# Optimization experiments

Measured on AMD Instinct MI355X. Metric: run time of the kernel, lower is better.

## Reference

```python
import jax, jax.numpy as jnp
import numpy as np

# Model constants matching init_kwargs
C1, C2, FS, IMG = 1024, 3, 16, 128
NF = FS * FS                     # n_features = 256 (== pos_out_dim)
L = C1 // NF                     # 4 hypernetwork-generated layers
WD = NF + (L - 1) * NF + L       # weight_dim = 1028
M = NF // 4                      # 64 frequencies per coord dim
SIGMA = 10.0
B = 8


def _coords_pe(b):
    """get_coords([IMG, IMG]) + positional_encoding, flattened to [b, IMG*IMG, NF]."""
    v0, v1 = -0.99999, 1.0
    r = (v1 - v0) / (2 * IMG)
    seq = v0 + r + 2 * r * jnp.arange(IMG, dtype=jnp.float32)
    gy, gx = jnp.meshgrid(seq, seq, indexing='ij')
    coords = jnp.stack([gy, gx], axis=-1)                 # [IMG, IMG, 2]
    j = jnp.arange(M, dtype=jnp.float32)
    coeffs = 2.0 * jnp.pi * (SIGMA ** (j / M))            # [M]
    vp = coeffs * coords[..., None]                       # [IMG, IMG, 2, M]
    pe = jnp.concatenate([jnp.cos(vp), jnp.sin(vp)], -1)  # [IMG, IMG, 2, 2M]
    pe = pe.reshape(IMG, IMG, 4 * M)                      # flatten(-2,-1)
    x2 = pe.reshape(1, IMG * IMG, NF)
    return jnp.broadcast_to(x2, (b, IMG * IMG, NF))


def setup_inputs() -> dict:
    key = jax.random.key(0)
    ks = jax.random.split(key, 5)
    std = 0.001  # matches _initialize_weights
    x = jax.random.normal(ks[0], (B, C1, FS, FS), jnp.float32)
    conv_w = std * jax.random.normal(ks[1], (C1 + L, C1), jnp.float32)  # 1x1 conv kernel
    conv_b = jnp.zeros((C1 + L,), jnp.float32)
    wfine_w = std * jax.random.normal(ks[2], (NF, NF), jnp.float32)
    wfine_b = jnp.zeros((NF,), jnp.float32)
    last1_w = std * jax.random.normal(ks[3], (C2, NF), jnp.float32)
    last1_b = jnp.zeros((C2,), jnp.float32)
    prelu_a = jnp.array(0.25, jnp.float32)  # nn.PReLU default single param
    return {"x": x, "conv_w": conv_w, "conv_b": conv_b,
            "wfine_w": wfine_w, "wfine_b": wfine_b,
            "last1_w": last1_w, "last1_b": last1_b, "prelu_a": prelu_a}


def reference(x, conv_w, conv_b, wfine_w, wfine_b, last1_w, last1_b, prelu_a):
    b = x.shape[0]
    x2 = _coords_pe(b)  # [b, N_px, NF]
    # 1x1 conv == channel matmul
    x1 = jnp.einsum('bchw,oc->bohw', x, conv_w) + conv_b[None, :, None, None]
    W = x1.reshape(b, WD, NF)
    W = jnp.einsum('bik,jk->bij', W, wfine_w) + wfine_b  # W_fine linear
    out = x2
    for j in range(L):
        wj = W[:, NF * j + j: NF * (j + 1) + j, :]           # [b, NF, NF]
        bj = W[:, NF * (j + 1) + j: NF * (j + 1) + j + 1, :]  # [b, 1, NF]
        h = jnp.einsum('bij,bjk->bik', out, wj) + bj
        out = jnp.where(h >= 0, h, prelu_a * h)              # PReLU
    out = jnp.einsum('bik,ck->bic', out, last1_w) + last1_b  # last1
    out = jax.nn.silu(out)                                   # SiLU
    out = out.transpose(0, 2, 1).reshape(b, C2, IMG, IMG)
    return out
```

## Files before the change

### kernel.cpp

```cpp
#include <hip/hip_runtime.h>
#include <hip/hip_fp16.h>
#include <math.h>

typedef _Float16 f16;
typedef _Float16 f16x4 __attribute__((ext_vector_type(4)));
typedef _Float16 f16x8 __attribute__((ext_vector_type(8)));
typedef float f32x4 __attribute__((ext_vector_type(4)));

#define MFMA16(a, b, c) __builtin_amdgcn_mfma_f32_16x16x32_f16((a), (b), (c), 0, 0, 0)

static constexpr float SW_W   = 1024.f;
static constexpr float SA_A   = 64.f;
static constexpr float SA1_s  = 16.f;
static constexpr float INV_SW    = 1.f / 1024.f;
static constexpr float INV_SASW  = 1.f / (64.f * 1024.f);
static constexpr float INV_SA1SW = 1.f / (16.f * 1024.f);

static constexpr size_t OFF_CY = 0;
static constexpr size_t OFF_CX = OFF_CY + 128 * 128 * 4;
static constexpr size_t OFF_LW = OFF_CX + 128 * 128 * 4;
static constexpr size_t OFF_XT = OFF_LW + 16 * 256 * 2;
static constexpr size_t OFF_X1 = OFF_XT + (size_t)8 * 256 * 1024 * 2;
static constexpr size_t OFF_W  = OFF_X1 + (size_t)8 * 1028 * 256 * 2;
static constexpr size_t OFF_AY = OFF_W  + (size_t)8 * 1028 * 256 * 4;
static constexpr size_t OFF_BX = OFF_AY + (size_t)8 * 128 * 256 * 2;
static constexpr size_t OFF_WT = OFF_BX + (size_t)8 * 128 * 256 * 2;

static __device__ inline f32x4 zero4() { f32x4 v = {0.f, 0.f, 0.f, 0.f}; return v; }

__global__ void k_prep(const float* __restrict__ x, f16* __restrict__ xT,
                       float* __restrict__ cy, float* __restrict__ cx,
                       f16* __restrict__ lwf, const float* __restrict__ lw)
{
    __shared__ float tile[64][65];
    const int bid = blockIdx.x;
    const int t = threadIdx.x;
    if (bid < 512) {
        const int b = bid >> 6;
        const int ct = (bid >> 2) & 15;
        const int nt = bid & 3;
        const int c0 = ct << 6, n0 = nt << 6;
        for (int i = 0; i < 16; i++) {
            int e = i * 256 + t;
            int cc = e >> 6, nn = e & 63;
            tile[cc][nn] = x[(size_t)((b << 10) + c0 + cc) * 256 + n0 + nn];
        }
        __syncthreads();
        for (int i = 0; i < 16; i++) {
            int e = i * 256 + t;
            int nn = e >> 6, cc = e & 63;
            xT[(size_t)((b << 8) + n0 + nn) * 1024 + c0 + cc] = (f16)tile[cc][nn];
        }
        return;
    }
    int id = (bid - 512) * 256 + t;
    const float r = 1.99999f / 256.f;
    if (id < 32768) {
        float* dst = (id < 16384) ? cy : cx;
        int e = id & 16383;
        int row = e >> 7, f = e & 127;
        float s = -0.99999f + r + 2.f * r * (float)row;
        float coef = 6.283185307179586f * powf(10.f, (float)(f & 63) * (1.f / 64.f));
        float arg = coef * s;
        dst[e] = (f < 64) ? cosf(arg) : sinf(arg);
    } else if (id < 33280) {
        int id2 = id - 32768;
        int c = id2 >> 6, lane = id2 & 63;
        int nlo = lane & 15, q4 = lane >> 4;
        f16x8 v;
        #pragma unroll
        for (int ko = 0; ko < 8; ko++)
            v[ko] = (nlo < 3) ? (f16)(lw[nlo * 256 + (c << 5) + (q4 << 3) + ko] * SW_W) : (f16)0.f;
        *(f16x8*)(lwf + id2 * 8) = v;
    }
}

template <int MODE>
__global__ __launch_bounds__(256, 4) void k_gemm(
    const float* __restrict__ Af32, const f16* __restrict__ Af16,
    const f16* __restrict__ Bf16, const float* __restrict__ Bf32,
    f16* __restrict__ out16, float* __restrict__ outW,
    const float* __restrict__ bias)
{
    constexpr int NC = MODE ? 8 : 32;
    __shared__ __align__(16) f16 Ab[2][64 * 32];
    __shared__ __align__(16) f16 Bb[2][64 * 32];
    const int t = threadIdx.x;
    const int lane = t & 63;
    const int wc = t >> 6;
    const int nlo = lane & 15, q4 = lane >> 4;
    const int blk = blockIdx.x;
    const int b = blk / 68;
    const int rem = blk % 68;
    const int m0 = (rem >> 2) << 6;
    const int n0 = (rem & 3) << 6;
    const int srow = t >> 2, sk = (t & 3) << 3;

    auto stageA = [&](int buf, int k0) {
        const int m = m0 + srow;
        f16x8 v;
        if (m < 1028) {
            if constexpr (MODE == 0) {
                const float* src = Af32 + (size_t)m * 1024 + k0 + sk;
                #pragma unroll
                for (int i = 0; i < 8; i++) v[i] = (f16)(src[i] * SW_W);
            } else {
                v = *(const f16x8*)(Af16 + (size_t)(b * 1028 + m) * 256 + k0 + sk);
            }
        } else {
            #pragma unroll
            for (int i = 0; i < 8; i++) v[i] = (f16)0.f;
        }
        *(f16x8*)(&Ab[buf][t << 3]) = v;
    };
    auto stageB = [&](int buf, int k0) {
        const int n = n0 + srow;
        f16x8 v;
        if constexpr (MODE == 0) {
            v = *(const f16x8*)(Bf16 + (size_t)((b << 8) + n) * 1024 + k0 + sk);
        } else {
            const float* src = Bf32 + (size_t)n * 256 + k0 + sk;
            #pragma unroll
            for (int i = 0; i < 8; i++) v[i] = (f16)(src[i] * SW_W);
        }
        *(f16x8*)(&Bb[buf][t << 3]) = v;
    };

    f32x4 acc[4];
    #pragma unroll
    for (int mt = 0; mt < 4; mt++) acc[mt] = zero4();

    stageA(0, 0); stageB(0, 0);
    __syncthreads();
    for (int c = 0; c < NC; c++) {
        const int cb = c & 1;
        if (c + 1 < NC) { stageA(cb ^ 1, (c + 1) << 5); stageB(cb ^ 1, (c + 1) << 5); }
        f16x8 af[4], bf;
        bf = *(const f16x8*)(&Bb[cb][(((wc << 4) + nlo) << 5) + (q4 << 3)]);
        #pragma unroll
        for (int mt = 0; mt < 4; mt++)
            af[mt] = *(const f16x8*)(&Ab[cb][(((mt << 4) + nlo) << 5) + (q4 << 3)]);
        #pragma unroll
        for (int mt = 0; mt < 4; mt++)
            acc[mt] = MFMA16(af[mt], bf, acc[mt]);
        __syncthreads();
    }
    const int nn = n0 + (wc << 4) + nlo;
    #pragma unroll
    for (int mt = 0; mt < 4; mt++) {
        #pragma unroll
        for (int i = 0; i < 4; i++) {
            const int m = m0 + (mt << 4) + (q4 << 2) + i;
            if (m < 1028) {
                if constexpr (MODE == 0) {
                    float v = (acc[mt][i] * INV_SW + bias[m]) * SA1_s;
                    out16[(size_t)(b * 1028 + m) * 256 + nn] = (f16)v;
                } else {
                    outW[(size_t)(b * 1028 + m) * 256 + nn] =
                        acc[mt][i] * INV_SA1SW + bias[nn];
                }
            }
        }
    }
}

__global__ void k_wprep(const float* __restrict__ cy, const float* __restrict__ cx,
                        const float* __restrict__ W, f16* __restrict__ ayF,
                        f16* __restrict__ bxF, f16* __restrict__ wjT)
{
    __shared__ float tile[64][65];
    const int bid = blockIdx.x;
    const int t = threadIdx.x;
    if (bid < 256) {
        const int b = bid >> 5, which = (bid >> 4) & 1, rtile = bid & 15;
        const int r0 = rtile << 3;
        const float* ctab = which ? cx : cy;
        const float* Wb = W + (size_t)(b * 1028 + (which ? 128 : 0)) * 256;
        float acc[8];
        #pragma unroll
        for (int r = 0; r < 8; r++) acc[r] = 0.f;
        for (int k = 0; k < 128; k++) {
            const float wv = Wb[(k << 8) + t];
            #pragma unroll
            for (int r = 0; r < 8; r++)
                acc[r] = fmaf(ctab[((r0 + r) << 7) + k], wv, acc[r]);
        }
        const float b1v = which ? 0.f : W[(size_t)(b * 1028 + 256) * 256 + t];
        f16* dst = which ? bxF : ayF;
        for (int r = 0; r < 8; r++)
            dst[(size_t)((b << 7) + r0 + r) * 256 + t] = (f16)((acc[r] + b1v) * SA_A);
        return;
    }
    const int id = bid - 256;
    const int b = id / 48;
    const int rr = id % 48;
    const int jj = rr / 16;
    const int tt = rr % 16;
    const int kt = tt >> 2, wt = tt & 3;
    const int k0 = kt << 6, n0 = wt << 6;
    const float* src = W + (size_t)(b * 1028 + 257 * (jj + 1)) * 256;
    for (int i = 0; i < 16; i++) {
        int e = i * 256 + t;
        int kk = e >> 6, nn = e & 63;
        tile[kk][nn] = src[(size_t)(k0 + kk) * 256 + n0 + nn];
    }
    __syncthreads();
    f16* dst = wjT + (size_t)(b * 3 + jj) * 65536;
    #pragma unroll
    for (int i = 0; i < 2; i++) {
        const int g = i * 256 + t;
        const int c_rel = g >> 8, sub = g & 255;
        const int nt = sub >> 6, ln = sub & 63;
        const int nl = ln & 15, q4g = ln >> 4;
        f16x8 v;
        #pragma unroll
        for (int ko = 0; ko < 8; ko++)
            v[ko] = (f16)(tile[(c_rel << 5) + (q4g << 3) + ko][(nt << 4) + nl] * SW_W);
        const int c = (kt << 1) + c_rel;
        *(f16x8*)(dst + (size_t)(((((c << 2) | wt) << 2) | nt) << 9) + (ln << 3)) = v;
    }
}

__global__ __launch_bounds__(256, 3) void k_main(
    const f16* __restrict__ wjT, const float* __restrict__ Wfull,
    const f16* __restrict__ ayF, const f16* __restrict__ bxF,
    const f16* __restrict__ lwf, const float* __restrict__ lb,
    const float* __restrict__ pa_p, float* __restrict__ out)
{
    __shared__ __align__(16) unsigned char actS[32768];
    const int t = threadIdx.x;
    const int lane = t & 63;
    const int wc = t >> 6;
    const int nlo = lane & 15, q4 = lane >> 4;
    const int blk = blockIdx.x;
    const int b = blk & 7, rt = blk >> 3;
    const int p0 = rt << 6;
    const int y = p0 >> 7, x0 = p0 & 127;
    const float pa = pa_p[0];

    {
        const int r = t & 63, g = t >> 6;
        const f16* ayr = ayF + (size_t)((b << 7) + y) * 256;
        const f16* bxr = bxF + (size_t)((b << 7) + x0 + r) * 256;
        const int rx = r & 7;
        #pragma unroll
        for (int mm = 0; mm < 8; mm++) {
            const int slot = (g << 3) + mm;
            const int f0 = slot << 3;
            f16x8 av = *(const f16x8*)(ayr + f0);
            f16x8 bv = *(const f16x8*)(bxr + f0);
            f16x8 v;
            #pragma unroll
            for (int i = 0; i < 8; i++) {
                float hv = (float)av[i] + (float)bv[i];
                hv = fmaxf(hv, 0.f) + pa * fminf(hv, 0.f);
                v[i] = (f16)hv;
            }
            *(f16x8*)(actS + (r << 9) + ((slot ^ rx) << 4)) = v;
        }
    }
    __syncthreads();

    for (int jj = 0; jj < 3; jj++) {
        const f16* wl = wjT + (size_t)(b * 3 + jj) * 65536;
        auto loadB = [&](f16x8* dstv, int c) {
            const f16* p = wl + (size_t)(((c << 2) | wc) << 11) + (lane << 3);
            #pragma unroll
            for (int nt = 0; nt < 4; nt++)
                dstv[nt] = *(const f16x8*)(p + (nt << 9));
        };
        f32x4 acc[4][4];
        #pragma unroll
        for (int pt = 0; pt < 4; pt++)
            #pragma unroll
            for (int nt = 0; nt < 4; nt++) acc[pt][nt] = zero4();

        f16x8 bfA[4], bfB[4];
        loadB(bfA, 0);
        #pragma unroll
        for (int c = 0; c < 8; c++) {
            f16x8* cur = (c & 1) ? bfB : bfA;
            f16x8* nxt = (c & 1) ? bfA : bfB;
            if (c < 7) loadB(nxt, c + 1);
            const int sl = (c << 2) + q4;
            f16x8 af[4];
            #pragma unroll
            for (int pt = 0; pt < 4; pt++) {
                const int rr = (pt << 4) + nlo;
                af[pt] = *(const f16x8*)(actS + (rr << 9) + ((sl ^ (rr & 7)) << 4));
            }
            #pragma unroll
            for (int pt = 0; pt < 4; pt++)
                #pragma unroll
                for (int nt = 0; nt < 4; nt++)
                    acc[pt][nt] = MFMA16(cur[nt], af[pt], acc[pt][nt]);
        }
        __syncthreads();

        const float* bias = Wfull + (size_t)(b * 1028 + 257 * (jj + 1) + 256) * 256;
        #pragma unroll
        for (int nt = 0; nt < 4; nt++) {
            const int nb = (wc << 6) + (nt << 4) + (q4 << 2);
            const f32x4 b4 = *(const f32x4*)(bias + nb);
            #pragma unroll
            for (int pt = 0; pt < 4; pt++) {
                const int rr = (pt << 4) + nlo;
                f16x4 pk;
                #pragma unroll
                for (int i = 0; i < 4; i++) {
                    float v = acc[pt][nt][i] * INV_SW + b4[i] * SA_A;
                    v = fmaxf(v, 0.f) + pa * fminf(v, 0.f);
                    pk[i] = (f16)v;
                }
                *(f16x4*)(actS + (rr << 9) + (((nb >> 3) ^ (rr & 7)) << 4) + ((nb & 7) << 1)) = pk;
            }
        }
        __syncthreads();
    }

    {
        f32x4 acc2 = zero4();
        const int rr = (wc << 4) + nlo;
        #pragma unroll
        for (int c = 0; c < 8; c++) {
            const int sl = (c << 2) + q4;
            const f16x8 af = *(const f16x8*)(actS + (rr << 9) + ((sl ^ (rr & 7)) << 4));
            const f16x8 lf = *(const f16x8*)(lwf + (((c << 6) + lane) << 3));
            acc2 = MFMA16(af, lf, acc2);
        }
        if (nlo < 3) {
            const float lbv = lb[nlo];
            float* ob = out + ((size_t)(b * 3 + nlo) << 14) + p0 + (wc << 4) + (q4 << 2);
            #pragma unroll
            for (int i = 0; i < 4; i++) {
                float z = acc2[i] * INV_SASW + lbv;
                ob[i] = z / (1.f + expf(-z));
            }
        }
    }
}

extern "C" void kernel_launch(void* const* d_in, const int* in_sizes, int n_in,
                              void* d_out, int out_size, void* d_ws, size_t ws_size,
                              hipStream_t stream)
{
    (void)in_sizes; (void)n_in; (void)out_size; (void)ws_size;
    const float* x       = (const float*)d_in[0];
    const float* conv_w  = (const float*)d_in[1];
    const float* conv_b  = (const float*)d_in[2];
    const float* wfine_w = (const float*)d_in[3];
    const float* wfine_b = (const float*)d_in[4];
    const float* last1_w = (const float*)d_in[5];
    const float* last1_b = (const float*)d_in[6];
    const float* prelu_a = (const float*)d_in[7];
    char* ws = (char*)d_ws;
    float* Cy  = (float*)(ws + OFF_CY);
    float* Cx  = (float*)(ws + OFF_CX);
    f16*   lwf = (f16*)(ws + OFF_LW);
    f16*   xT  = (f16*)(ws + OFF_XT);
    f16*   x1  = (f16*)(ws + OFF_X1);
    float* W   = (float*)(ws + OFF_W);
    f16*   AyF = (f16*)(ws + OFF_AY);
    f16*   BxF = (f16*)(ws + OFF_BX);
    f16*   wjT = (f16*)(ws + OFF_WT);

    k_prep<<<642, 256, 0, stream>>>(x, xT, Cy, Cx, lwf, last1_w);
    k_gemm<0><<<544, 256, 0, stream>>>(conv_w, nullptr, xT, nullptr, x1, nullptr, conv_b);
    k_gemm<1><<<544, 256, 0, stream>>>(nullptr, x1, nullptr, wfine_w, nullptr, W, wfine_b);
    k_wprep<<<640, 256, 0, stream>>>(Cy, Cx, W, AyF, BxF, wjT);
    k_main<<<2048, 256, 0, stream>>>(wjT, W, AyF, BxF, lwf, last1_b, prelu_a, (float*)d_out);
}
```

Before: 124.2 us.

## Fuse conv and W_fine GEMMs into one kernel with pre-converted fp16 weights

Merges the two GEMM kernels into one k_fused kernel. Each block computes a 64-row by 256-column x1 tile, keeps it in shared memory, and applies W_fine directly, so the x1 intermediate never goes to global memory. conv_w and wfine_w are converted to fp16 once in k_prep (wfine_w in MFMA fragment layout), which removes per-tile fp32 conversion. In k_main, the weight prefetch now runs across layer boundaries and the bias loads are hoisted. The catch is that the fused kernel launches only 136 blocks on a large GPU, so parallelism is low and each block does more serial work.

Measured after the change: 114.2 us. 1.09x faster.

```diff
diff --git a/kernel.cpp b/kernel.cpp
--- a/kernel.cpp
+++ b/kernel.cpp
@@ -20,8 +20,9 @@
 static constexpr size_t OFF_CX = OFF_CY + 128 * 128 * 4;
 static constexpr size_t OFF_LW = OFF_CX + 128 * 128 * 4;
 static constexpr size_t OFF_XT = OFF_LW + 16 * 256 * 2;
-static constexpr size_t OFF_X1 = OFF_XT + (size_t)8 * 256 * 1024 * 2;
-static constexpr size_t OFF_W  = OFF_X1 + (size_t)8 * 1028 * 256 * 2;
+static constexpr size_t OFF_CW = OFF_XT + (size_t)8 * 256 * 1024 * 2;
+static constexpr size_t OFF_WF = OFF_CW + (size_t)1088 * 1024 * 2;
+static constexpr size_t OFF_W  = OFF_WF + 256 * 256 * 2;
 static constexpr size_t OFF_AY = OFF_W  + (size_t)8 * 1028 * 256 * 4;
 static constexpr size_t OFF_BX = OFF_AY + (size_t)8 * 128 * 256 * 2;
 static constexpr size_t OFF_WT = OFF_BX + (size_t)8 * 128 * 256 * 2;
@@ -30,7 +31,9 @@
 
 __global__ void k_prep(const float* __restrict__ x, f16* __restrict__ xT,
                        float* __restrict__ cy, float* __restrict__ cx,
-                       f16* __restrict__ lwf, const float* __restrict__ lw)
+                       f16* __restrict__ lwf, const float* __restrict__ lw,
+                       const float* __restrict__ cw, f16* __restrict__ cw16,
+                       const float* __restrict__ wf, f16* __restrict__ wf16)
 {
     __shared__ float tile[64][65];
     const int bid = blockIdx.x;
@@ -53,112 +56,174 @@
         }
         return;
     }
-    int id = (bid - 512) * 256 + t;
-    const float r = 1.99999f / 256.f;
-    if (id < 32768) {
-        float* dst = (id < 16384) ? cy : cx;
-        int e = id & 16383;
-        int row = e >> 7, f = e & 127;
-        float s = -0.99999f + r + 2.f * r * (float)row;
-        float coef = 6.283185307179586f * powf(10.f, (float)(f & 63) * (1.f / 64.f));
-        float arg = coef * s;
-        dst[e] = (f < 64) ? cosf(arg) : sinf(arg);
-    } else if (id < 33280) {
-        int id2 = id - 32768;
-        int c = id2 >> 6, lane = id2 & 63;
-        int nlo = lane & 15, q4 = lane >> 4;
+    if (bid < 642) {
+        int id = (bid - 512) * 256 + t;
+        const float r = 1.99999f / 256.f;
+        if (id < 32768) {
+            float* dst = (id < 16384) ? cy : cx;
+            int e = id & 16383;
+            int row = e >> 7, f = e & 127;
+            float s = -0.99999f + r + 2.f * r * (float)row;
+            float coef = 6.283185307179586f * powf(10.f, (float)(f & 63) * (1.f / 64.f));
+            float arg = coef * s;
+            dst[e] = (f < 64) ? cosf(arg) : sinf(arg);
+        } else if (id < 33280) {
+            int id2 = id - 32768;
+            int c = id2 >> 6, lane = id2 & 63;
+            int nlo = lane & 15, q4 = lane >> 4;
+            f16x8 v;
+            #pragma unroll
+            for (int ko = 0; ko < 8; ko++)
+                v[ko] = (nlo < 3) ? (f16)(lw[nlo * 256 + (c << 5) + (q4 << 3) + ko] * SW_W) : (f16)0.f;
+            *(f16x8*)(lwf + id2 * 8) = v;
+        }
+        return;
+    }
+    if (bid < 1186) {
+        const int g8 = (bid - 642) * 256 + t;
+        const int row = g8 >> 7, col0 = (g8 & 127) << 3;
         f16x8 v;
+        if (row < 1028) {
+            const float* src = cw + (size_t)row * 1024 + col0;
+            #pragma unroll
+            for (int i = 0; i < 8; i++) v[i] = (f16)(src[i] * SW_W);
+        } else {
+            #pragma unroll
+            for (int i = 0; i < 8; i++) v[i] = (f16)0.f;
+        }
+        *(f16x8*)(cw16 + (size_t)g8 * 8) = v;
+        return;
+    }
+    {
+        const int gg = (bid - 1186) * 256 + t;
+        const int lane = gg & 63, nt = (gg >> 6) & 3, wt = (gg >> 8) & 3, c = gg >> 10;
+        const int nlo = lane & 15, q4 = lane >> 4;
+        const int n = (wt << 6) + (nt << 4) + nlo;
+        f16x8 v;
         #pragma unroll
         for (int ko = 0; ko < 8; ko++)
-            v[ko] = (nlo < 3) ? (f16)(lw[nlo * 256 + (c << 5) + (q4 << 3) + ko] * SW_W) : (f16)0.f;
-        *(f16x8*)(lwf + id2 * 8) = v;
+            v[ko] = (f16)(wf[(size_t)n * 256 + (c << 5) + (q4 << 3) + ko] * SW_W);
+        *(f16x8*)(wf16 + (size_t)gg * 8) = v;
     }
 }
 
-template <int MODE>
-__global__ __launch_bounds__(256, 4) void k_gemm(
-    const float* __restrict__ Af32, const f16* __restrict__ Af16,
-    const f16* __restrict__ Bf16, const float* __restrict__ Bf32,
-    f16* __restrict__ out16, float* __restrict__ outW,
-    const float* __restrict__ bias)
+__global__ __launch_bounds__(256, 2) void k_fused(
+    const f16* __restrict__ cw16, const f16* __restrict__ xT,
+    const f16* __restrict__ wf16, const float* __restrict__ conv_b,
+    const float* __restrict__ wfine_b, float* __restrict__ W)
 {
-    constexpr int NC = MODE ? 8 : 32;
     __shared__ __align__(16) f16 Ab[2][64 * 32];
-    __shared__ __align__(16) f16 Bb[2][64 * 32];
+    __shared__ __align__(16) f16 Bb[2][256 * 32];
+    __shared__ __align__(16) unsigned char x1S[32768];
     const int t = threadIdx.x;
     const int lane = t & 63;
     const int wc = t >> 6;
     const int nlo = lane & 15, q4 = lane >> 4;
-    const int blk = blockIdx.x;
-    const int b = blk / 68;
-    const int rem = blk % 68;
-    const int m0 = (rem >> 2) << 6;
-    const int n0 = (rem & 3) << 6;
-    const int srow = t >> 2, sk = (t & 3) << 3;
+    const int b = blockIdx.x & 7, mtile = blockIdx.x >> 3;
+    const int m0 = mtile << 6;
 
     auto stageA = [&](int buf, int k0) {
-        const int m = m0 + srow;
-        f16x8 v;
-        if (m < 1028) {
-            if constexpr (MODE == 0) {
-                const float* src = Af32 + (size_t)m * 1024 + k0 + sk;
-                #pragma unroll
-                for (int i = 0; i < 8; i++) v[i] = (f16)(src[i] * SW_W);
-            } else {
-                v = *(const f16x8*)(Af16 + (size_t)(b * 1028 + m) * 256 + k0 + sk);
-            }
-        } else {
-            #pragma unroll
-            for (int i = 0; i < 8; i++) v[i] = (f16)0.f;
-        }
-        *(f16x8*)(&Ab[buf][t << 3]) = v;
+        *(f16x8*)(&Ab[buf][t << 3]) =
+            *(const f16x8*)(cw16 + (size_t)(m0 + (t >> 2)) * 1024 + k0 + ((t & 3) << 3));
     };
     auto stageB = [&](int buf, int k0) {
-        const int n = n0 + srow;
-        f16x8 v;
-        if constexpr (MODE == 0) {
-            v = *(const f16x8*)(Bf16 + (size_t)((b << 8) + n) * 1024 + k0 + sk);
-        } else {
-            const float* src = Bf32 + (size_t)n * 256 + k0 + sk;
-            #pragma unroll
-            for (int i = 0; i < 8; i++) v[i] = (f16)(src[i] * SW_W);
-        }
-        *(f16x8*)(&Bb[buf][t << 3]) = v;
+        #pragma unroll
+        for (int i = 0; i < 4; i++)
+            *(f16x8*)(&Bb[buf][(i * 256 + t) << 3]) =
+                *(const f16x8*)(xT + (size_t)((b << 8) + (i << 6) + (t >> 2)) * 1024 + k0 + ((t & 3) << 3));
     };
 
-    f32x4 acc[4];
+    f32x4 acc1[4][4];
     #pragma unroll
-    for (int mt = 0; mt < 4; mt++) acc[mt] = zero4();
+    for (int pt = 0; pt < 4; pt++)
+        #pragma unroll
+        for (int mc = 0; mc < 4; mc++) acc1[pt][mc] = zero4();
 
     stageA(0, 0); stageB(0, 0);
     __syncthreads();
-    for (int c = 0; c < NC; c++) {
+    for (int c = 0; c < 32; c++) {
         const int cb = c & 1;
-        if (c + 1 < NC) { stageA(cb ^ 1, (c + 1) << 5); stageB(cb ^ 1, (c + 1) << 5); }
-        f16x8 af[4], bf;
-        bf = *(const f16x8*)(&Bb[cb][(((wc << 4) + nlo) << 5) + (q4 << 3)]);
-        #pragma unroll
-        for (int mt = 0; mt < 4; mt++)
-            af[mt] = *(const f16x8*)(&Ab[cb][(((mt << 4) + nlo) << 5) + (q4 << 3)]);
-        #pragma unroll
-        for (int mt = 0; mt < 4; mt++)
-            acc[mt] = MFMA16(af[mt], bf, acc[mt]);
+        if (c + 1 < 32) { stageA(cb ^ 1, (c + 1) << 5); stageB(cb ^ 1, (c + 1) << 5); }
+        f16x8 bf[4], af[4];
+        #pragma unroll
+        for (int pt = 0; pt < 4; pt++)
+            bf[pt] = *(const f16x8*)(&Bb[cb][((wc << 8) + (((pt << 4) + nlo) << 2) + q4) << 3]);
+        #pragma unroll
+        for (int mc = 0; mc < 4; mc++)
+            af[mc] = *(const f16x8*)(&Ab[cb][(((((mc << 4) + nlo) << 2) + q4)) << 3]);
+        #pragma unroll
+        for (int pt = 0; pt < 4; pt++)
+            #pragma unroll
+            for (int mc = 0; mc < 4; mc++)
+                acc1[pt][mc] = MFMA16(bf[pt], af[mc], acc1[pt][mc]);
         __syncthreads();
     }
-    const int nn = n0 + (wc << 4) + nlo;
+
+    {
+        float cbv[4];
+        #pragma unroll
+        for (int mc = 0; mc < 4; mc++) {
+            const int m = m0 + (mc << 4) + nlo;
+            cbv[mc] = (m < 1028) ? conv_b[m] : 0.f;
+        }
+        #pragma unroll
+        for (int pt = 0; pt < 4; pt++) {
+            const int p0 = (wc << 6) + (pt << 4) + (q4 << 2);
+            #pragma unroll
+            for (int mc = 0; mc < 4; mc++) {
+                const int r = (mc << 4) + nlo;
+                f16x4 pk;
+                #pragma unroll
+                for (int i = 0; i < 4; i++)
+                    pk[i] = (f16)((acc1[pt][mc][i] * INV_SW + cbv[mc]) * SA1_s);
+                *(f16x4*)(x1S + (r << 9) + (((p0 >> 3) ^ (r & 7)) << 4) + ((p0 & 7) << 1)) = pk;
+            }
+        }
+    }
+    __syncthreads();
+
+    f32x4 acc2[4][4];
     #pragma unroll
-    for (int mt = 0; mt < 4; mt++) {
-        #pragma unroll
-        for (int i = 0; i < 4; i++) {
-            const int m = m0 + (mt << 4) + (q4 << 2) + i;
+    for (int mc = 0; mc < 4; mc++)
+        #pragma unroll
+        for (int jt = 0; jt < 4; jt++) acc2[mc][jt] = zero4();
+
+    auto loadW = [&](f16x8* d, int c2) {
+        const f16* p = wf16 + (size_t)((((c2 << 2) | wc)) << 11) + (lane << 3);
+        #pragma unroll
+        for (int jt = 0; jt < 4; jt++) d[jt] = *(const f16x8*)(p + (jt << 9));
+    };
+    f16x8 wfA[4], wfB[4];
+    loadW(wfA, 0);
+    #pragma unroll
+    for (int c2 = 0; c2 < 8; c2++) {
+        f16x8* cur = (c2 & 1) ? wfB : wfA;
+        f16x8* nxt = (c2 & 1) ? wfA : wfB;
+        if (c2 < 7) loadW(nxt, c2 + 1);
+        f16x8 af2[4];
+        #pragma unroll
+        for (int mc = 0; mc < 4; mc++) {
+            const int r = (mc << 4) + nlo;
+            af2[mc] = *(const f16x8*)(x1S + (r << 9) + ((((c2 << 2) + q4) ^ (r & 7)) << 4));
+        }
+        #pragma unroll
+        for (int mc = 0; mc < 4; mc++)
+            #pragma unroll
+            for (int jt = 0; jt < 4; jt++)
+                acc2[mc][jt] = MFMA16(cur[jt], af2[mc], acc2[mc][jt]);
+    }
+    #pragma unroll
+    for (int jt = 0; jt < 4; jt++) {
+        const int j0 = (wc << 6) + (jt << 4) + (q4 << 2);
+        const f32x4 b4 = *(const f32x4*)(wfine_b + j0);
+        #pragma unroll
+        for (int mc = 0; mc < 4; mc++) {
+            const int m = m0 + (mc << 4) + nlo;
             if (m < 1028) {
-                if constexpr (MODE == 0) {
-                    float v = (acc[mt][i] * INV_SW + bias[m]) * SA1_s;
-                    out16[(size_t)(b * 1028 + m) * 256 + nn] = (f16)v;
-                } else {
-                    outW[(size_t)(b * 1028 + m) * 256 + nn] =
-                        acc[mt][i] * INV_SA1SW + bias[nn];
-                }
+                f32x4 o;
+                #pragma unroll
+                for (int i = 0; i < 4; i++) o[i] = acc2[mc][jt][i] * INV_SA1SW + b4[i];
+                *(f32x4*)(W + ((size_t)(b * 1028 + m) << 8) + j0) = o;
             }
         }
     }
@@ -238,6 +303,16 @@
     const int y = p0 >> 7, x0 = p0 & 127;
     const float pa = pa_p[0];
 
+    const f16* wl0 = wjT + (size_t)(b * 3) * 65536;
+    auto loadBg = [&](f16x8* dstv, int g) {
+        const f16* p = wl0 + (size_t)(g >> 3) * 65536 + ((size_t)((((g & 7) << 2) | wc)) << 11) + (lane << 3);
+        #pragma unroll
+        for (int nt = 0; nt < 4; nt++) dstv[nt] = *(const f16x8*)(p + (nt << 9));
+    };
+
+    f16x8 bfA[4], bfB[4];
+    loadBg(bfA, 0);
+
     {
         const int r = t & 63, g = t >> 6;
         const f16* ayr = ayF + (size_t)((b << 7) + y) * 256;
@@ -262,26 +337,24 @@
     __syncthreads();
 
     for (int jj = 0; jj < 3; jj++) {
-        const f16* wl = wjT + (size_t)(b * 3 + jj) * 65536;
-        auto loadB = [&](f16x8* dstv, int c) {
-            const f16* p = wl + (size_t)(((c << 2) | wc) << 11) + (lane << 3);
-            #pragma unroll
-            for (int nt = 0; nt < 4; nt++)
-                dstv[nt] = *(const f16x8*)(p + (nt << 9));
-        };
+        const float* bias = Wfull + (size_t)(b * 1028 + 257 * (jj + 1) + 256) * 256;
+        f32x4 bias4[4];
+        #pragma unroll
+        for (int nt = 0; nt < 4; nt++)
+            bias4[nt] = *(const f32x4*)(bias + (wc << 6) + (nt << 4) + (q4 << 2));
+
         f32x4 acc[4][4];
         #pragma unroll
         for (int pt = 0; pt < 4; pt++)
             #pragma unroll
             for (int nt = 0; nt < 4; nt++) acc[pt][nt] = zero4();
 
-        f16x8 bfA[4], bfB[4];
-        loadB(bfA, 0);
         #pragma unroll
         for (int c = 0; c < 8; c++) {
-            f16x8* cur = (c & 1) ? bfB : bfA;
-            f16x8* nxt = (c & 1) ? bfA : bfB;
-            if (c < 7) loadB(nxt, c + 1);
+            const int g = jj * 8 + c;
+            f16x8* cur = (g & 1) ? bfB : bfA;
+            f16x8* nxt = (g & 1) ? bfA : bfB;
+            if (g < 23) loadBg(nxt, g + 1);
             const int sl = (c << 2) + q4;
             f16x8 af[4];
             #pragma unroll
@@ -297,18 +370,16 @@
         }
         __syncthreads();
 
-        const float* bias = Wfull + (size_t)(b * 1028 + 257 * (jj + 1) + 256) * 256;
         #pragma unroll
         for (int nt = 0; nt < 4; nt++) {
             const int nb = (wc << 6) + (nt << 4) + (q4 << 2);
-            const f32x4 b4 = *(const f32x4*)(bias + nb);
             #pragma unroll
             for (int pt = 0; pt < 4; pt++) {
                 const int rr = (pt << 4) + nlo;
                 f16x4 pk;
                 #pragma unroll
                 for (int i = 0; i < 4; i++) {
-                    float v = acc[pt][nt][i] * INV_SW + b4[i] * SA_A;
+                    float v = acc[pt][nt][i] * INV_SW + bias4[nt][i] * SA_A;
                     v = fmaxf(v, 0.f) + pa * fminf(v, 0.f);
                     pk[i] = (f16)v;
                 }
@@ -358,15 +429,15 @@
     float* Cx  = (float*)(ws + OFF_CX);
     f16*   lwf = (f16*)(ws + OFF_LW);
     f16*   xT  = (f16*)(ws + OFF_XT);
-    f16*   x1  = (f16*)(ws + OFF_X1);
+    f16*   cw16= (f16*)(ws + OFF_CW);
+    f16*   wf16= (f16*)(ws + OFF_WF);
     float* W   = (float*)(ws + OFF_W);
     f16*   AyF = (f16*)(ws + OFF_AY);
     f16*   BxF = (f16*)(ws + OFF_BX);
     f16*   wjT = (f16*)(ws + OFF_WT);
 
-    k_prep<<<642, 256, 0, stream>>>(x, xT, Cy, Cx, lwf, last1_w);
-    k_gemm<0><<<544, 256, 0, stream>>>(conv_w, nullptr, xT, nullptr, x1, nullptr, conv_b);
-    k_gemm<1><<<544, 256, 0, stream>>>(nullptr, x1, nullptr, wfine_w, nullptr, W, wfine_b);
+    k_prep<<<1218, 256, 0, stream>>>(x, xT, Cy, Cx, lwf, last1_w, conv_w, cw16, wfine_w, wf16);
+    k_fused<<<136, 256, 0, stream>>>(cw16, xT, wf16, conv_b, wfine_b, W);
     k_wprep<<<640, 256, 0, stream>>>(Cy, Cx, W, AyF, BxF, wjT);
     k_main<<<2048, 256, 0, stream>>>(wjT, W, AyF, BxF, lwf, last1_b, prelu_a, (float*)d_out);
 }
```

## Reassociate conv and W_fine GEMMs, prefetch weights across layers in main kernel

Applied to the files above, without the earlier changes.

The two front GEMMs are reassociated as conv_w·(x·wfine_wᵀ) instead of (conv_w·x)·wfine_wᵀ. The per-batch x·wfine product is computed first, and the bias term is folded in analytically as conv_b·rowsum(wfine) + wfine_b. This removes the x transpose pass and lets the weights be converted to f16 once in the prep kernel. In the main kernel, hypernetwork weight fragments are now prefetched across layer boundaries, activation fragments from LDS are double-buffered, and MFMA blocks are wrapped in s_setprio. The intermediate is rounded to f16 without a scale factor, which risks precision loss, and the extra register buffers may reduce occupancy.

Measured after the change: 143.9 us. 1.16x slower.

```diff
diff --git a/kernel.cpp b/kernel.cpp
--- a/kernel.cpp
+++ b/kernel.cpp
@@ -9,80 +9,94 @@
 
 #define MFMA16(a, b, c) __builtin_amdgcn_mfma_f32_16x16x32_f16((a), (b), (c), 0, 0, 0)
 
-static constexpr float SW_W   = 1024.f;
-static constexpr float SA_A   = 64.f;
-static constexpr float SA1_s  = 16.f;
-static constexpr float INV_SW    = 1.f / 1024.f;
-static constexpr float INV_SASW  = 1.f / (64.f * 1024.f);
-static constexpr float INV_SA1SW = 1.f / (16.f * 1024.f);
+static constexpr float SW_W    = 1024.f;
+static constexpr float SA_A    = 64.f;
+static constexpr float INV_SW  = 1.f / 1024.f;
+static constexpr float INV_SW2 = 1.f / (1024.f * 1024.f);
+static constexpr float INV_SASW = 1.f / (64.f * 1024.f);
 
 static constexpr size_t OFF_CY = 0;
-static constexpr size_t OFF_CX = OFF_CY + 128 * 128 * 4;
-static constexpr size_t OFF_LW = OFF_CX + 128 * 128 * 4;
-static constexpr size_t OFF_XT = OFF_LW + 16 * 256 * 2;
-static constexpr size_t OFF_X1 = OFF_XT + (size_t)8 * 256 * 1024 * 2;
-static constexpr size_t OFF_W  = OFF_X1 + (size_t)8 * 1028 * 256 * 2;
+static constexpr size_t OFF_CX = OFF_CY + 65536;
+static constexpr size_t OFF_LW = OFF_CX + 65536;
+static constexpr size_t OFF_S  = OFF_LW + 8192;
+static constexpr size_t OFF_CW = OFF_S  + 1024;
+static constexpr size_t OFF_WF = OFF_CW + (size_t)1088 * 1024 * 2;
+static constexpr size_t OFF_M2 = OFF_WF + 131072;
+static constexpr size_t OFF_W  = OFF_M2 + (size_t)8 * 256 * 1024 * 2;
 static constexpr size_t OFF_AY = OFF_W  + (size_t)8 * 1028 * 256 * 4;
 static constexpr size_t OFF_BX = OFF_AY + (size_t)8 * 128 * 256 * 2;
 static constexpr size_t OFF_WT = OFF_BX + (size_t)8 * 128 * 256 * 2;
 
 static __device__ inline f32x4 zero4() { f32x4 v = {0.f, 0.f, 0.f, 0.f}; return v; }
 
-__global__ void k_prep(const float* __restrict__ x, f16* __restrict__ xT,
-                       float* __restrict__ cy, float* __restrict__ cx,
-                       f16* __restrict__ lwf, const float* __restrict__ lw)
-{
-    __shared__ float tile[64][65];
+__global__ void k_prep(float* __restrict__ cy, float* __restrict__ cx,
+                       f16* __restrict__ lwf, const float* __restrict__ lw,
+                       const float* __restrict__ cw, f16* __restrict__ cw16,
+                       const float* __restrict__ wf, f16* __restrict__ wf16,
+                       float* __restrict__ S)
+{
     const int bid = blockIdx.x;
     const int t = threadIdx.x;
-    if (bid < 512) {
-        const int b = bid >> 6;
-        const int ct = (bid >> 2) & 15;
-        const int nt = bid & 3;
-        const int c0 = ct << 6, n0 = nt << 6;
-        for (int i = 0; i < 16; i++) {
-            int e = i * 256 + t;
-            int cc = e >> 6, nn = e & 63;
-            tile[cc][nn] = x[(size_t)((b << 10) + c0 + cc) * 256 + n0 + nn];
-        }
-        __syncthreads();
-        for (int i = 0; i < 16; i++) {
-            int e = i * 256 + t;
-            int nn = e >> 6, cc = e & 63;
-            xT[(size_t)((b << 8) + n0 + nn) * 1024 + c0 + cc] = (f16)tile[cc][nn];
+    if (bid < 130) {
+        int id = bid * 256 + t;
+        const float r = 1.99999f / 256.f;
+        if (id < 32768) {
+            float* dst = (id < 16384) ? cy : cx;
+            int e = id & 16383;
+            int row = e >> 7, f = e & 127;
+            float s = -0.99999f + r + 2.f * r * (float)row;
+            float coef = 6.283185307179586f * powf(10.f, (float)(f & 63) * (1.f / 64.f));
+            float arg = coef * s;
+            dst[e] = (f < 64) ? cosf(arg) : sinf(arg);
+        } else {
+            int id2 = id - 32768;
+            int c = id2 >> 6, lane = id2 & 63;
+            int nlo = lane & 15, q4 = lane >> 4;
+            f16x8 v;
+            #pragma unroll
+            for (int ko = 0; ko < 8; ko++)
+                v[ko] = (nlo < 3) ? (f16)(lw[nlo * 256 + (c << 5) + (q4 << 3) + ko] * SW_W) : (f16)0.f;
+            *(f16x8*)(lwf + id2 * 8) = v;
         }
         return;
     }
-    int id = (bid - 512) * 256 + t;
-    const float r = 1.99999f / 256.f;
-    if (id < 32768) {
-        float* dst = (id < 16384) ? cy : cx;
-        int e = id & 16383;
-        int row = e >> 7, f = e & 127;
-        float s = -0.99999f + r + 2.f * r * (float)row;
-        float coef = 6.283185307179586f * powf(10.f, (float)(f & 63) * (1.f / 64.f));
-        float arg = coef * s;
-        dst[e] = (f < 64) ? cosf(arg) : sinf(arg);
-    } else if (id < 33280) {
-        int id2 = id - 32768;
-        int c = id2 >> 6, lane = id2 & 63;
-        int nlo = lane & 15, q4 = lane >> 4;
+    if (bid < 674) {
+        const int g8 = (bid - 130) * 256 + t;
+        const int row = g8 >> 7, col0 = (g8 & 127) << 3;
         f16x8 v;
-        #pragma unroll
-        for (int ko = 0; ko < 8; ko++)
-            v[ko] = (nlo < 3) ? (f16)(lw[nlo * 256 + (c << 5) + (q4 << 3) + ko] * SW_W) : (f16)0.f;
-        *(f16x8*)(lwf + id2 * 8) = v;
-    }
-}
-
-template <int MODE>
-__global__ __launch_bounds__(256, 4) void k_gemm(
-    const float* __restrict__ Af32, const f16* __restrict__ Af16,
-    const f16* __restrict__ Bf16, const float* __restrict__ Bf32,
-    f16* __restrict__ out16, float* __restrict__ outW,
-    const float* __restrict__ bias)
-{
-    constexpr int NC = MODE ? 8 : 32;
+        if (row < 1028) {
+            const float* src = cw + (size_t)row * 1024 + col0;
+            #pragma unroll
+            for (int i = 0; i < 8; i++) v[i] = (f16)(src[i] * SW_W);
+        } else {
+            #pragma unroll
+            for (int i = 0; i < 8; i++) v[i] = (f16)0.f;
+        }
+        *(f16x8*)(cw16 + (size_t)g8 * 8) = v;
+        return;
+    }
+    if (bid < 706) {
+        const int gg = (bid - 674) * 256 + t;
+        const int row = gg >> 5, col0 = (gg & 31) << 3;
+        const float* src = wf + (size_t)row * 256 + col0;
+        f16x8 v;
+        #pragma unroll
+        for (int i = 0; i < 8; i++) v[i] = (f16)(src[i] * SW_W);
+        *(f16x8*)(wf16 + (size_t)gg * 8) = v;
+        return;
+    }
+    {
+        const float* src = wf + (size_t)t * 256;
+        float s = 0.f;
+        for (int k = 0; k < 256; k++) s += src[k];
+        S[t] = s;
+    }
+}
+
+__global__ __launch_bounds__(256, 4) void k_gemmA(
+    const float* __restrict__ x, const f16* __restrict__ wf16,
+    f16* __restrict__ M2)
+{
     __shared__ __align__(16) f16 Ab[2][64 * 32];
     __shared__ __align__(16) f16 Bb[2][64 * 32];
     const int t = threadIdx.x;
@@ -90,40 +104,20 @@
     const int wc = t >> 6;
     const int nlo = lane & 15, q4 = lane >> 4;
     const int blk = blockIdx.x;
-    const int b = blk / 68;
-    const int rem = blk % 68;
-    const int m0 = (rem >> 2) << 6;
-    const int n0 = (rem & 3) << 6;
-    const int srow = t >> 2, sk = (t & 3) << 3;
+    const int b = blk >> 6, rem = blk & 63;
+    const int jt = rem >> 4, ct = rem & 15;
+    const int j0 = jt << 6, c0 = ct << 6;
 
     auto stageA = [&](int buf, int k0) {
-        const int m = m0 + srow;
+        const float* src = x + (((size_t)((b << 10) + c0 + (t >> 2))) << 8) + k0 + ((t & 3) << 3);
         f16x8 v;
-        if (m < 1028) {
-            if constexpr (MODE == 0) {
-                const float* src = Af32 + (size_t)m * 1024 + k0 + sk;
-                #pragma unroll
-                for (int i = 0; i < 8; i++) v[i] = (f16)(src[i] * SW_W);
-            } else {
-                v = *(const f16x8*)(Af16 + (size_t)(b * 1028 + m) * 256 + k0 + sk);
-            }
-        } else {
-            #pragma unroll
-            for (int i = 0; i < 8; i++) v[i] = (f16)0.f;
-        }
+        #pragma unroll
+        for (int i = 0; i < 8; i++) v[i] = (f16)src[i];
         *(f16x8*)(&Ab[buf][t << 3]) = v;
     };
     auto stageB = [&](int buf, int k0) {
-        const int n = n0 + srow;
-        f16x8 v;
-        if constexpr (MODE == 0) {
-            v = *(const f16x8*)(Bf16 + (size_t)((b << 8) + n) * 1024 + k0 + sk);
-        } else {
-            const float* src = Bf32 + (size_t)n * 256 + k0 + sk;
-            #pragma unroll
-            for (int i = 0; i < 8; i++) v[i] = (f16)(src[i] * SW_W);
-        }
-        *(f16x8*)(&Bb[buf][t << 3]) = v;
+        *(f16x8*)(&Bb[buf][t << 3]) =
+            *(const f16x8*)(wf16 + (((size_t)(j0 + (t >> 2))) << 8) + k0 + ((t & 3) << 3));
     };
 
     f32x4 acc[4];
@@ -132,9 +126,9 @@
 
     stageA(0, 0); stageB(0, 0);
     __syncthreads();
-    for (int c = 0; c < NC; c++) {
+    for (int c = 0; c < 8; c++) {
         const int cb = c & 1;
-        if (c + 1 < NC) { stageA(cb ^ 1, (c + 1) << 5); stageB(cb ^ 1, (c + 1) << 5); }
+        if (c + 1 < 8) { stageA(cb ^ 1, (c + 1) << 5); stageB(cb ^ 1, (c + 1) << 5); }
         f16x8 af[4], bf;
         bf = *(const f16x8*)(&Bb[cb][(((wc << 4) + nlo) << 5) + (q4 << 3)]);
         #pragma unroll
@@ -145,21 +139,74 @@
             acc[mt] = MFMA16(af[mt], bf, acc[mt]);
         __syncthreads();
     }
-    const int nn = n0 + (wc << 4) + nlo;
+    const int j = j0 + (wc << 4) + nlo;
     #pragma unroll
     for (int mt = 0; mt < 4; mt++) {
-        #pragma unroll
-        for (int i = 0; i < 4; i++) {
-            const int m = m0 + (mt << 4) + (q4 << 2) + i;
-            if (m < 1028) {
-                if constexpr (MODE == 0) {
-                    float v = (acc[mt][i] * INV_SW + bias[m]) * SA1_s;
-                    out16[(size_t)(b * 1028 + m) * 256 + nn] = (f16)v;
-                } else {
-                    outW[(size_t)(b * 1028 + m) * 256 + nn] =
-                        acc[mt][i] * INV_SA1SW + bias[nn];
-                }
-            }
+        const int cc = c0 + (mt << 4) + (q4 << 2);
+        f16x4 pk;
+        #pragma unroll
+        for (int i = 0; i < 4; i++) pk[i] = (f16)acc[mt][i];
+        *(f16x4*)(M2 + (((size_t)((b << 8) + j)) << 10) + cc) = pk;
+    }
+}
+
+__global__ __launch_bounds__(256, 4) void k_gemmB(
+    const f16* __restrict__ cw16, const f16* __restrict__ M2,
+    const float* __restrict__ conv_b, const float* __restrict__ S,
+    const float* __restrict__ wfine_b, float* __restrict__ W)
+{
+    __shared__ __align__(16) f16 Ab[2][64 * 32];
+    __shared__ __align__(16) f16 Bb[2][64 * 32];
+    const int t = threadIdx.x;
+    const int lane = t & 63;
+    const int wc = t >> 6;
+    const int nlo = lane & 15, q4 = lane >> 4;
+    const int blk = blockIdx.x;
+    const int b = blk / 68, rem = blk % 68;
+    const int it = rem >> 2, jt = rem & 3;
+    const int i0 = it << 6, j0 = jt << 6;
+
+    auto stageA = [&](int buf, int k0) {
+        *(f16x8*)(&Ab[buf][t << 3]) =
+            *(const f16x8*)(M2 + (((size_t)((b << 8) + j0 + (t >> 2))) << 10) + k0 + ((t & 3) << 3));
+    };
+    auto stageB = [&](int buf, int k0) {
+        *(f16x8*)(&Bb[buf][t << 3]) =
+            *(const f16x8*)(cw16 + (((size_t)(i0 + (t >> 2))) << 10) + k0 + ((t & 3) << 3));
+    };
+
+    f32x4 acc[4];
+    #pragma unroll
+    for (int mt = 0; mt < 4; mt++) acc[mt] = zero4();
+
+    stageA(0, 0); stageB(0, 0);
+    __syncthreads();
+    for (int c = 0; c < 32; c++) {
+        const int cb = c & 1;
+        if (c + 1 < 32) { stageA(cb ^ 1, (c + 1) << 5); stageB(cb ^ 1, (c + 1) << 5); }
+        f16x8 af[4], bf;
+        bf = *(const f16x8*)(&Bb[cb][(((wc << 4) + nlo) << 5) + (q4 << 3)]);
+        #pragma unroll
+        for (int mt = 0; mt < 4; mt++)
+            af[mt] = *(const f16x8*)(&Ab[cb][(((mt << 4) + nlo) << 5) + (q4 << 3)]);
+        #pragma unroll
+        for (int mt = 0; mt < 4; mt++)
+            acc[mt] = MFMA16(af[mt], bf, acc[mt]);
+        __syncthreads();
+    }
+    const int i = i0 + (wc << 4) + nlo;
+    if (i < 1028) {
+        const float cbv = conv_b[i];
+        #pragma unroll
+        for (int mt = 0; mt < 4; mt++) {
+            const int j = j0 + (mt << 4) + (q4 << 2);
+            const f32x4 sv = *(const f32x4*)(S + j);
+            const f32x4 wb = *(const f32x4*)(wfine_b + j);
+            f32x4 o;
+            #pragma unroll
+            for (int ii = 0; ii < 4; ii++)
+                o[ii] = acc[mt][ii] * INV_SW2 + cbv * sv[ii] + wb[ii];
+            *(f32x4*)(W + (((size_t)(b * 1028 + i)) << 8) + j) = o;
         }
     }
 }
@@ -238,6 +285,24 @@
     const int y = p0 >> 7, x0 = p0 & 127;
     const float pa = pa_p[0];
 
+    const f16* wl0 = wjT + (size_t)(b * 3) * 65536;
+    auto loadBg = [&](f16x8* dstv, int g) {
+        const f16* p = wl0 + (size_t)(g >> 3) * 65536 + ((size_t)((((g & 7) << 2) | wc)) << 11) + (lane << 3);
+        #pragma unroll
+        for (int nt = 0; nt < 4; nt++) dstv[nt] = *(const f16x8*)(p + (nt << 9));
+    };
+    auto readAf = [&](f16x8* dstv, int c) {
+        const int sl = (c << 2) + q4;
+        #pragma unroll
+        for (int pt = 0; pt < 4; pt++) {
+            const int rr = (pt << 4) + nlo;
+            dstv[pt] = *(const f16x8*)(actS + (rr << 9) + ((sl ^ (rr & 7)) << 4));
+        }
+    };
+
+    f16x8 bfA[4], bfB[4];
+    loadBg(bfA, 0);
+
     {
         const int r = t & 63, g = t >> 6;
         const f16* ayr = ayF + (size_t)((b << 7) + y) * 256;
@@ -262,53 +327,51 @@
     __syncthreads();
 
     for (int jj = 0; jj < 3; jj++) {
-        const f16* wl = wjT + (size_t)(b * 3 + jj) * 65536;
-        auto loadB = [&](f16x8* dstv, int c) {
-            const f16* p = wl + (size_t)(((c << 2) | wc) << 11) + (lane << 3);
-            #pragma unroll
-            for (int nt = 0; nt < 4; nt++)
-                dstv[nt] = *(const f16x8*)(p + (nt << 9));
-        };
+        const float* bias = Wfull + (size_t)(b * 1028 + 257 * (jj + 1) + 256) * 256;
+        f32x4 bias4[4];
+        #pragma unroll
+        for (int nt = 0; nt < 4; nt++) {
+            bias4[nt] = *(const f32x4*)(bias + (wc << 6) + (nt << 4) + (q4 << 2));
+            bias4[nt] *= SA_A;
+        }
+
         f32x4 acc[4][4];
         #pragma unroll
         for (int pt = 0; pt < 4; pt++)
             #pragma unroll
             for (int nt = 0; nt < 4; nt++) acc[pt][nt] = zero4();
 
-        f16x8 bfA[4], bfB[4];
-        loadB(bfA, 0);
+        f16x8 afA[4], afB[4];
+        readAf(afA, 0);
         #pragma unroll
         for (int c = 0; c < 8; c++) {
-            f16x8* cur = (c & 1) ? bfB : bfA;
-            f16x8* nxt = (c & 1) ? bfA : bfB;
-            if (c < 7) loadB(nxt, c + 1);
-            const int sl = (c << 2) + q4;
-            f16x8 af[4];
-            #pragma unroll
-            for (int pt = 0; pt < 4; pt++) {
-                const int rr = (pt << 4) + nlo;
-                af[pt] = *(const f16x8*)(actS + (rr << 9) + ((sl ^ (rr & 7)) << 4));
-            }
+            const int g = jj * 8 + c;
+            f16x8* curW = (g & 1) ? bfB : bfA;
+            f16x8* nxtW = (g & 1) ? bfA : bfB;
+            f16x8* curA = (c & 1) ? afB : afA;
+            f16x8* nxtA = (c & 1) ? afA : afB;
+            if (g < 23) loadBg(nxtW, g + 1);
+            if (c < 7)  readAf(nxtA, c + 1);
+            __builtin_amdgcn_s_setprio(1);
             #pragma unroll
             for (int pt = 0; pt < 4; pt++)
                 #pragma unroll
                 for (int nt = 0; nt < 4; nt++)
-                    acc[pt][nt] = MFMA16(cur[nt], af[pt], acc[pt][nt]);
+                    acc[pt][nt] = MFMA16(curW[nt], curA[pt], acc[pt][nt]);
+            __builtin_amdgcn_s_setprio(0);
         }
         __syncthreads();
 
-        const float* bias = Wfull + (size_t)(b * 1028 + 257 * (jj + 1) + 256) * 256;
         #pragma unroll
         for (int nt = 0; nt < 4; nt++) {
             const int nb = (wc << 6) + (nt << 4) + (q4 << 2);
-            const f32x4 b4 = *(const f32x4*)(bias + nb);
             #pragma unroll
             for (int pt = 0; pt < 4; pt++) {
                 const int rr = (pt << 4) + nlo;
                 f16x4 pk;
                 #pragma unroll
                 for (int i = 0; i < 4; i++) {
-                    float v = acc[pt][nt][i] * INV_SW + b4[i] * SA_A;
+                    float v = fmaf(acc[pt][nt][i], INV_SW, bias4[nt][i]);
                     v = fmaxf(v, 0.f) + pa * fminf(v, 0.f);
                     pk[i] = (f16)v;
                 }
@@ -357,16 +420,18 @@
     float* Cy  = (float*)(ws + OFF_CY);
     float* Cx  = (float*)(ws + OFF_CX);
     f16*   lwf = (f16*)(ws + OFF_LW);
-    f16*   xT  = (f16*)(ws + OFF_XT);
-    f16*   x1  = (f16*)(ws + OFF_X1);
+    float* S   = (float*)(ws + OFF_S);
+    f16*   cw16= (f16*)(ws + OFF_CW);
+    f16*   wf16= (f16*)(ws + OFF_WF);
+    f16*   M2  = (f16*)(ws + OFF_M2);
     float* W   = (float*)(ws + OFF_W);
     f16*   AyF = (f16*)(ws + OFF_AY);
     f16*   BxF = (f16*)(ws + OFF_BX);
     f16*   wjT = (f16*)(ws + OFF_WT);
 
-    k_prep<<<642, 256, 0, stream>>>(x, xT, Cy, Cx, lwf, last1_w);
-    k_gemm<0><<<544, 256, 0, stream>>>(conv_w, nullptr, xT, nullptr, x1, nullptr, conv_b);
-    k_gemm<1><<<544, 256, 0, stream>>>(nullptr, x1, nullptr, wfine_w, nullptr, W, wfine_b);
+    k_prep<<<707, 256, 0, stream>>>(Cy, Cx, lwf, last1_w, conv_w, cw16, wfine_w, wf16, S);
+    k_gemmA<<<512, 256, 0, stream>>>(x, wf16, M2);
+    k_gemmB<<<544, 256, 0, stream>>>(cw16, M2, conv_b, S, wfine_b, W);
     k_wprep<<<640, 256, 0, stream>>>(Cy, Cx, W, AyF, BxF, wjT);
     k_main<<<2048, 256, 0, stream>>>(wjT, W, AyF, BxF, lwf, last1_b, prelu_a, (float*)d_out);
 }
```
